# Kernel tuning notes

Measured on AMD Instinct MI355X. Metric: run time of the kernel, lower is better.

The kernel has to match this reference:

```python
import jax, jax.numpy as jnp
import numpy as np

WARMUP = 5

def _smooth_l1(x):
    a = jnp.abs(x)
    return jnp.where(a < 1.0, 0.5 * a * a, a - 0.5)


def setup_inputs() -> dict:
    key = jax.random.key(0)
    ks = jax.random.split(key, 6)
    B, S, N, M, C = 8, 4, 8192, 50, 10
    return dict(
        pred_boxes=jax.random.normal(ks[0], (B, S, N, 7), jnp.float32),
        pred_classes=jax.random.normal(ks[1], (B, S, N, C), jnp.float32),
        pred_scores=jax.random.normal(ks[2], (B, S, N), jnp.float32),
        gt_boxes=jax.random.normal(ks[3], (B, M, 7), jnp.float32) * 3.0,
        gt_classes=jax.random.randint(ks[4], (B, M), 0, C),
        n_gt=jax.random.randint(ks[5], (B,), 1, M + 1),
        w_center=jnp.float32(2.0),   # loss_weights['center']
        w_obj=jnp.float32(0.5),      # loss_weights['obj']
        w_unmatched=jnp.float32(5.0),# loss_weights['unmatched']
        epoch=0,
    )


def _forward(pred_boxes, pred_classes, pred_scores, gt_boxes, gt_classes, n_gt, w_center, w_obj, w_unmatched, epoch):
    # epoch < WARMUP path: k_factor=10, use_objectness=False, distance_threshold=5.0, cls_weight=0
    K_FACTOR = 10
    COST_THRESH = 5.0 * 10.0  # distance_threshold * 10
    B, S, N, _ = pred_boxes.shape
    M = gt_boxes.shape[1]
    gt_mask = jnp.arange(M)[None, :] < n_gt[:, None]            # [B,M] valid (non-padded) GTs

    pc = pred_boxes[..., :3]                                    # [B,S,N,3]
    gc = gt_boxes[..., :3]                                      # [B,M,3]
    diff = pc[:, :, :, None, :] - gc[:, None, None, :, :]       # [B,S,N,M,3]
    dist = jnp.sqrt(jnp.sum(diff * diff, axis=-1))              # [B,S,N,M] center L2 cost

    # ---- progressive matching (vectorized over B,S,GT) ----
    cost = jnp.where(gt_mask[:, None, None, :], dist, jnp.inf)
    masked = jnp.where(cost < COST_THRESH, cost, jnp.inf)
    neg = -jnp.swapaxes(masked, -1, -2)                         # [B,S,M,N]
    vals, idx = jax.lax.top_k(neg, K_FACTOR)                    # k smallest costs per gt
    pick_ok = vals > -jnp.inf                                   # [B,S,M,k] valid picks
    gt_ids = jnp.broadcast_to(jnp.arange(M, dtype=jnp.int32)[None, None, :, None], idx.shape)
    bidx = jnp.broadcast_to(jnp.arange(B)[:, None, None, None], idx.shape)
    sidx = jnp.broadcast_to(jnp.arange(S)[None, :, None, None], idx.shape)
    assign = jnp.full((B, S, N), -1, dtype=jnp.int32)
    assign = assign.at[bidx, sidx, idx].max(jnp.where(pick_ok, gt_ids, -1))
    matched_gt = pick_ok.any(-1)                                # [B,S,M]
    unmatched = gt_mask[:, None, :] & ~matched_gt               # [B,S,M]

    # ---- center loss (smooth-L1 over matched query/GT center pairs) ----
    pos = assign >= 0                                           # [B,S,N]
    a = jnp.maximum(assign, 0)
    gtc = gc[jnp.arange(B)[:, None, None], a]                   # [B,S,N,3]
    n_pos = pos.sum().astype(jnp.float32)
    loss_center = jnp.sum(_smooth_l1(pc - gtc) * pos[..., None]) / jnp.maximum(n_pos * 3.0, 1.0)

    # ---- progressive objectness loss (BCE-with-logits + dynamic pos_weight) ----
    t = pos.astype(pred_scores.dtype)
    n_neg = jnp.float32(t.size) - n_pos
    pw = jnp.minimum(10.0, n_neg / jnp.maximum(n_pos, 1.0))     # epoch < warmup branch
    x = pred_scores
    loss_obj = jnp.mean(pw * t * jax.nn.softplus(-x) + (1.0 - t) * jax.nn.softplus(x))

    # ---- unmatched-GT loss: pull 5 nearest predictions toward each unmatched GT ----
    dist_t = jnp.swapaxes(dist, -1, -2)                         # [B,S,M,N]
    nd, ni = jax.lax.top_k(-dist_t, 5)
    nd = -nd                                                    # 5 smallest distances [B,S,M,5]
    b5 = jnp.broadcast_to(jnp.arange(B)[:, None, None, None], ni.shape)
    s5 = jnp.broadcast_to(jnp.arange(S)[None, :, None, None], ni.shape)
    obj5 = pred_scores[b5, s5, ni]                              # [B,S,M,5]
    per_gt = jnp.mean(jnp.exp(-nd / 2.0) * (1.0 - obj5), axis=-1)
    per_gt = jnp.where(unmatched, per_gt, 0.0)
    n_entries = jnp.sum(unmatched.any(-1)).astype(jnp.float32)  # number of (b,s) pairs with unmatched gts
    loss_unm = per_gt.sum() / jnp.maximum(n_entries, 1.0)

    return loss_center * w_center + loss_obj * w_obj + loss_unm * w_unmatched


def reference(pred_boxes, pred_classes, pred_scores, gt_boxes, gt_classes, n_gt, w_center, w_obj, w_unmatched, epoch):
    return _forward(pred_boxes, pred_classes, pred_scores, gt_boxes, gt_classes, n_gt, w_center, w_obj, w_unmatched, epoch)
```

## Files before the change

kernel.cpp:

```cpp
#include <hip/hip_runtime.h>

#define NB 8
#define NS 4
#define NN 8192
#define NM 50
#define K10 10
#define THREADS 256
#define COST_THRESH 50.0f
#define LOSS_BLOCKS 256
#define NBUCK 1024
#define CAP 256
#define TOTAL (NB * NS * NN)

__device__ __forceinline__ bool lexless(float d1, int i1, float d2, int i2) {
  return (d1 < d2) || (d1 == d2 && i1 < i2);
}

__global__ void __launch_bounds__(256) prep_kernel(
    const float* __restrict__ pred_boxes, float* __restrict__ packed,
    int* __restrict__ assign, float* __restrict__ acc,
    int* __restrict__ bs_unm, int* __restrict__ done) {
  int i = blockIdx.x * blockDim.x + threadIdx.x;
  for (int j = i; j < TOTAL; j += gridDim.x * blockDim.x) {
    assign[j] = -1;
    packed[j] = pred_boxes[j * 7 + 0];
    packed[TOTAL + j] = pred_boxes[j * 7 + 1];
    packed[2 * TOTAL + j] = pred_boxes[j * 7 + 2];
  }
  if (i == 0) { acc[0] = 0.0f; *done = 0; }
  if (i >= 64 && i < 64 + NB * NS) bs_unm[i - 64] = 0;
}

__global__ void __launch_bounds__(256) topk_kernel(
    const float* __restrict__ packed, const float* __restrict__ pred_scores,
    const float* __restrict__ gt_boxes, const int* __restrict__ n_gt,
    int* __restrict__ assign, float* __restrict__ per_gt_sum,
    int* __restrict__ bs_unm) {
  const int blk = blockIdx.x;
  const int m = blk % NM;
  const int bs = blk / NM;
  const int b = bs / NS;
  const int t = threadIdx.x;

  __shared__ float sd2[NN];
  __shared__ int shist[NBUCK];
  __shared__ float scd[CAP];
  __shared__ int sci[CAP];
  __shared__ float sred[16];
  __shared__ float sbb[2];
  __shared__ int scnt;
  __shared__ int sbucket;
  __shared__ float soutd[K10];
  __shared__ int souti[K10];

  for (int i = t; i < NBUCK; i += THREADS) shist[i] = 0;
  if (t == 0) { scnt = 0; sbucket = NBUCK - 2; }

  const float gx = gt_boxes[(b * NM + m) * 7 + 0];
  const float gy = gt_boxes[(b * NM + m) * 7 + 1];
  const float gz = gt_boxes[(b * NM + m) * 7 + 2];
  const bool valid = (m < n_gt[b]);

  const float* px = packed + (size_t)bs * NN;
  const float* py = px + TOTAL;
  const float* pz = py + TOTAL;

  float lmin = INFINITY, lmax = 0.0f;
#pragma unroll
  for (int k = 0; k < NN / THREADS; k++) {
    int n = t + k * THREADS;
    float dx = px[n] - gx;
    float dy = py[n] - gy;
    float dz = pz[n] - gz;
    float d2 = dx * dx + dy * dy + dz * dz;
    sd2[n] = d2;
    lmin = fminf(lmin, d2);
    lmax = fmaxf(lmax, d2);
  }
#pragma unroll
  for (int off = 32; off >= 1; off >>= 1) {
    lmin = fminf(lmin, __shfl_down(lmin, off));
    lmax = fmaxf(lmax, __shfl_down(lmax, off));
  }
  int wave = t >> 6;
  if ((t & 63) == 0) { sred[wave] = lmin; sred[8 + wave] = lmax; }
  __syncthreads();
  if (t == 0) {
    float bmin = fminf(fminf(sred[0], sred[1]), fminf(sred[2], sred[3]));
    float bmax = fmaxf(fmaxf(sred[8], sred[9]), fmaxf(sred[10], sred[11]));
    sbb[0] = bmin;
    sbb[1] = (float)NBUCK / fmaxf(bmax - bmin, 1e-30f);
  }
  __syncthreads();
  const float bmin = sbb[0], scale = sbb[1];

#pragma unroll
  for (int k = 0; k < NN / THREADS; k++) {
    int n = t + k * THREADS;
    int bidx = (int)((sd2[n] - bmin) * scale);
    bidx = min(NBUCK - 1, max(0, bidx));
    atomicAdd(&shist[bidx], 1);
  }
  __syncthreads();

  if (t < 64) {
    int lsum = 0;
    for (int i = 0; i < NBUCK / 64; i++) lsum += shist[t * (NBUCK / 64) + i];
    int incl = lsum;
#pragma unroll
    for (int off = 1; off < 64; off <<= 1) {
      int v = __shfl_up(incl, off);
      if (t >= off) incl += v;
    }
    int excl = incl - lsum;
    if (excl < K10 && incl >= K10) {
      int c = excl;
      for (int i = 0; i < NBUCK / 64; i++) {
        c += shist[t * (NBUCK / 64) + i];
        if (c >= K10) { sbucket = t * (NBUCK / 64) + i; break; }
      }
    }
  }
  __syncthreads();
  const float bound = bmin + ((float)(sbucket + 2) + 0.5f) / scale;

#pragma unroll
  for (int k = 0; k < NN / THREADS; k++) {
    int n = t + k * THREADS;
    float d2 = sd2[n];
    if (d2 < bound) {
      int p = atomicAdd(&scnt, 1);
      if (p < CAP) { scd[p] = d2; sci[p] = n; }
    }
  }
  __syncthreads();
  const int K = min(scnt, CAP);

  for (int c = t; c < K; c += THREADS) scd[c] = sqrtf(scd[c]);
  __syncthreads();
  for (int c = t; c < K; c += THREADS) {
    float dc = scd[c];
    int ic = sci[c];
    int rank = 0;
    for (int o = 0; o < K; o++) rank += lexless(scd[o], sci[o], dc, ic) ? 1 : 0;
    if (rank < K10) { soutd[rank] = dc; souti[rank] = ic; }
  }
  __syncthreads();

  if (t < 64) {
    bool pick = (t < K10) && valid && (soutd[t] < COST_THRESH);
    if (pick) atomicMax(&assign[(size_t)bs * NN + souti[t]], m);
    bool matched = __any(pick);
    if (valid && !matched) {
      float a = 0.0f;
      if (t < 5) a = expf(-0.5f * soutd[t]) * (1.0f - pred_scores[(size_t)bs * NN + souti[t]]);
#pragma unroll
      for (int off = 8; off >= 1; off >>= 1) a += __shfl_down(a, off);
      if (t == 0) {
        atomicAdd(per_gt_sum, a * 0.2f);
        atomicOr(&bs_unm[bs], 1);
      }
    }
  }
}

__global__ void __launch_bounds__(256) loss_final_kernel(
    const float* __restrict__ packed, const float* __restrict__ pred_scores,
    const float* __restrict__ gt_boxes, const int* __restrict__ assign,
    float* __restrict__ partials, int* __restrict__ done,
    const float* __restrict__ acc, const int* __restrict__ bs_unm,
    const float* __restrict__ wc, const float* __restrict__ wo,
    const float* __restrict__ wu, float* __restrict__ out) {
  int tid = blockIdx.x * blockDim.x + threadIdx.x;
  float lc = 0.0f, spp = 0.0f, spn = 0.0f, np = 0.0f;
  for (int i = tid; i < TOTAL; i += gridDim.x * blockDim.x) {
    int a = assign[i];
    float x = pred_scores[i];
    if (a >= 0) {
      np += 1.0f;
      int b = i / (NS * NN);
      const float* gbp = &gt_boxes[(b * NM + a) * 7];
#pragma unroll
      for (int c = 0; c < 3; c++) {
        float diff = packed[c * TOTAL + i] - gbp[c];
        float ad = fabsf(diff);
        lc += (ad < 1.0f) ? 0.5f * ad * ad : (ad - 0.5f);
      }
      spp += log1pf(expf(-fabsf(x))) + fmaxf(-x, 0.0f);
    } else {
      spn += log1pf(expf(-fabsf(x))) + fmaxf(x, 0.0f);
    }
  }
#pragma unroll
  for (int off = 32; off >= 1; off >>= 1) {
    lc += __shfl_down(lc, off);
    spp += __shfl_down(spp, off);
    spn += __shfl_down(spn, off);
    np += __shfl_down(np, off);
  }
  __shared__ float red[4][4];
  __shared__ int s_last;
  int wave = threadIdx.x >> 6;
  if ((threadIdx.x & 63) == 0) {
    red[wave][0] = lc; red[wave][1] = spp; red[wave][2] = spn; red[wave][3] = np;
  }
  __syncthreads();
  if (threadIdx.x == 0) {
    float o0 = 0, o1 = 0, o2 = 0, o3 = 0;
#pragma unroll
    for (int w = 0; w < 4; w++) { o0 += red[w][0]; o1 += red[w][1]; o2 += red[w][2]; o3 += red[w][3]; }
    float* p = &partials[(size_t)blockIdx.x * 8];
    __hip_atomic_store(&p[0], o0, __ATOMIC_RELAXED, __HIP_MEMORY_SCOPE_AGENT);
    __hip_atomic_store(&p[1], o1, __ATOMIC_RELAXED, __HIP_MEMORY_SCOPE_AGENT);
    __hip_atomic_store(&p[2], o2, __ATOMIC_RELAXED, __HIP_MEMORY_SCOPE_AGENT);
    __hip_atomic_store(&p[3], o3, __ATOMIC_RELAXED, __HIP_MEMORY_SCOPE_AGENT);
    __threadfence();
    int ticket = __hip_atomic_fetch_add(done, 1, __ATOMIC_ACQ_REL, __HIP_MEMORY_SCOPE_AGENT);
    s_last = (ticket == gridDim.x - 1) ? 1 : 0;
  }
  __syncthreads();
  if (s_last) {
    __threadfence();
    const int t = threadIdx.x;
    float l0 = __hip_atomic_load(&partials[t * 8 + 0], __ATOMIC_RELAXED, __HIP_MEMORY_SCOPE_AGENT);
    float l1 = __hip_atomic_load(&partials[t * 8 + 1], __ATOMIC_RELAXED, __HIP_MEMORY_SCOPE_AGENT);
    float l2 = __hip_atomic_load(&partials[t * 8 + 2], __ATOMIC_RELAXED, __HIP_MEMORY_SCOPE_AGENT);
    float l3 = __hip_atomic_load(&partials[t * 8 + 3], __ATOMIC_RELAXED, __HIP_MEMORY_SCOPE_AGENT);
#pragma unroll
    for (int off = 32; off >= 1; off >>= 1) {
      l0 += __shfl_down(l0, off);
      l1 += __shfl_down(l1, off);
      l2 += __shfl_down(l2, off);
      l3 += __shfl_down(l3, off);
    }
    __shared__ float red2[4][4];
    if ((t & 63) == 0) {
      red2[t >> 6][0] = l0; red2[t >> 6][1] = l1; red2[t >> 6][2] = l2; red2[t >> 6][3] = l3;
    }
    __syncthreads();
    if (t == 0) {
      float o0 = 0, o1 = 0, o2 = 0, o3 = 0;
#pragma unroll
      for (int w = 0; w < 4; w++) { o0 += red2[w][0]; o1 += red2[w][1]; o2 += red2[w][2]; o3 += red2[w][3]; }
      int ne = 0;
      for (int i = 0; i < NB * NS; i++) ne += bs_unm[i];
      float n_pos = o3;
      float loss_center = o0 / fmaxf(n_pos * 3.0f, 1.0f);
      float n_neg = (float)TOTAL - n_pos;
      float pw = fminf(10.0f, n_neg / fmaxf(n_pos, 1.0f));
      float loss_obj = (pw * o1 + o2) / (float)TOTAL;
      float loss_unm = acc[0] / fmaxf((float)ne, 1.0f);
      out[0] = loss_center * wc[0] + loss_obj * wo[0] + loss_unm * wu[0];
    }
  }
}

extern "C" void kernel_launch(void* const* d_in, const int* in_sizes, int n_in,
                              void* d_out, int out_size, void* d_ws, size_t ws_size,
                              hipStream_t stream) {
  const float* pred_boxes = (const float*)d_in[0];
  const float* pred_scores = (const float*)d_in[2];
  const float* gt_boxes = (const float*)d_in[3];
  const int* n_gt = (const int*)d_in[5];
  const float* wc = (const float*)d_in[6];
  const float* wo = (const float*)d_in[7];
  const float* wu = (const float*)d_in[8];
  float* out = (float*)d_out;

  char* ws = (char*)d_ws;
  int* assign = (int*)ws;
  float* packed = (float*)(ws + (size_t)TOTAL * 4);
  float* acc = (float*)(ws + (size_t)TOTAL * 16);
  int* done = (int*)((char*)acc + 64);
  int* bs_unm = (int*)((char*)acc + 128);
  float* partials = (float*)((char*)acc + 512);

  prep_kernel<<<512, 256, 0, stream>>>(pred_boxes, packed, assign, acc, bs_unm, done);
  topk_kernel<<<NB * NS * NM, THREADS, 0, stream>>>(packed, pred_scores, gt_boxes,
                                                    n_gt, assign, &acc[0], bs_unm);
  loss_final_kernel<<<LOSS_BLOCKS, 256, 0, stream>>>(packed, pred_scores, gt_boxes, assign,
                                                     partials, done, acc, bs_unm, wc, wo, wu, out);
}
```

Baseline: 48.15 us.

## Keep distances in registers, vectorize loads, use 512 threads and sub-histograms

The top-k kernel now keeps per-thread squared distances in registers instead of a 32KB shared array, loads coordinates as float4, runs with 512 threads per block, and spreads histogram atomics over four per-wave sub-histograms that are merged before the prefix scan. This removes the large shared-memory footprint that limited occupancy and cuts atomic contention on the histogram. The cost is register pressure from 16 live distances per thread plus an extra merge pass and barrier. Candidate indices are recomputed from the float4 layout, and the final rank loop is unchanged.

```diff
diff --git a/kernel.cpp b/kernel.cpp
--- a/kernel.cpp
+++ b/kernel.cpp
@@ -5,12 +5,14 @@
 #define NN 8192
 #define NM 50
 #define K10 10
-#define THREADS 256
 #define COST_THRESH 50.0f
 #define LOSS_BLOCKS 256
 #define NBUCK 1024
+#define NSUB 4
 #define CAP 256
 #define TOTAL (NB * NS * NN)
+#define TT 512
+#define ELEMS (NN / TT)
 
 __device__ __forceinline__ bool lexless(float d1, int i1, float d2, int i2) {
   return (d1 < d2) || (d1 == d2 && i1 < i2);
@@ -31,7 +33,7 @@
   if (i >= 64 && i < 64 + NB * NS) bs_unm[i - 64] = 0;
 }
 
-__global__ void __launch_bounds__(256) topk_kernel(
+__global__ void __launch_bounds__(TT) topk_kernel(
     const float* __restrict__ packed, const float* __restrict__ pred_scores,
     const float* __restrict__ gt_boxes, const int* __restrict__ n_gt,
     int* __restrict__ assign, float* __restrict__ per_gt_sum,
@@ -42,8 +44,7 @@
   const int b = bs / NS;
   const int t = threadIdx.x;
 
-  __shared__ float sd2[NN];
-  __shared__ int shist[NBUCK];
+  __shared__ int shist[NSUB][NBUCK];
   __shared__ float scd[CAP];
   __shared__ int sci[CAP];
   __shared__ float sred[16];
@@ -53,7 +54,7 @@
   __shared__ float soutd[K10];
   __shared__ int souti[K10];
 
-  for (int i = t; i < NBUCK; i += THREADS) shist[i] = 0;
+  for (int i = t; i < NSUB * NBUCK; i += TT) ((int*)shist)[i] = 0;
   if (t == 0) { scnt = 0; sbucket = NBUCK - 2; }
 
   const float gx = gt_boxes[(b * NM + m) * 7 + 0];
@@ -61,51 +62,64 @@
   const float gz = gt_boxes[(b * NM + m) * 7 + 2];
   const bool valid = (m < n_gt[b]);
 
-  const float* px = packed + (size_t)bs * NN;
-  const float* py = px + TOTAL;
-  const float* pz = py + TOTAL;
-
+  const float4* px4 = (const float4*)(packed + (size_t)bs * NN);
+  const float4* py4 = (const float4*)(packed + TOTAL + (size_t)bs * NN);
+  const float4* pz4 = (const float4*)(packed + 2 * TOTAL + (size_t)bs * NN);
+
+  float d2r[ELEMS];
   float lmin = INFINITY, lmax = 0.0f;
 #pragma unroll
-  for (int k = 0; k < NN / THREADS; k++) {
-    int n = t + k * THREADS;
-    float dx = px[n] - gx;
-    float dy = py[n] - gy;
-    float dz = pz[n] - gz;
-    float d2 = dx * dx + dy * dy + dz * dz;
-    sd2[n] = d2;
-    lmin = fminf(lmin, d2);
-    lmax = fmaxf(lmax, d2);
+  for (int c = 0; c < ELEMS / 4; c++) {
+    float4 vx = px4[c * TT + t];
+    float4 vy = py4[c * TT + t];
+    float4 vz = pz4[c * TT + t];
+    float dx, dy, dz;
+    dx = vx.x - gx; dy = vy.x - gy; dz = vz.x - gz; d2r[c * 4 + 0] = dx * dx + dy * dy + dz * dz;
+    dx = vx.y - gx; dy = vy.y - gy; dz = vz.y - gz; d2r[c * 4 + 1] = dx * dx + dy * dy + dz * dz;
+    dx = vx.z - gx; dy = vy.z - gy; dz = vz.z - gz; d2r[c * 4 + 2] = dx * dx + dy * dy + dz * dz;
+    dx = vx.w - gx; dy = vy.w - gy; dz = vz.w - gz; d2r[c * 4 + 3] = dx * dx + dy * dy + dz * dz;
+#pragma unroll
+    for (int j = 0; j < 4; j++) {
+      lmin = fminf(lmin, d2r[c * 4 + j]);
+      lmax = fmaxf(lmax, d2r[c * 4 + j]);
+    }
   }
 #pragma unroll
   for (int off = 32; off >= 1; off >>= 1) {
     lmin = fminf(lmin, __shfl_down(lmin, off));
     lmax = fmaxf(lmax, __shfl_down(lmax, off));
   }
-  int wave = t >> 6;
+  const int wave = t >> 6;
   if ((t & 63) == 0) { sred[wave] = lmin; sred[8 + wave] = lmax; }
   __syncthreads();
   if (t == 0) {
-    float bmin = fminf(fminf(sred[0], sred[1]), fminf(sred[2], sred[3]));
-    float bmax = fmaxf(fmaxf(sred[8], sred[9]), fmaxf(sred[10], sred[11]));
+    float bmin = INFINITY, bmax = 0.0f;
+#pragma unroll
+    for (int w = 0; w < TT / 64; w++) {
+      bmin = fminf(bmin, sred[w]);
+      bmax = fmaxf(bmax, sred[8 + w]);
+    }
     sbb[0] = bmin;
     sbb[1] = (float)NBUCK / fmaxf(bmax - bmin, 1e-30f);
   }
   __syncthreads();
   const float bmin = sbb[0], scale = sbb[1];
 
-#pragma unroll
-  for (int k = 0; k < NN / THREADS; k++) {
-    int n = t + k * THREADS;
-    int bidx = (int)((sd2[n] - bmin) * scale);
+  int* hist = shist[wave & (NSUB - 1)];
+#pragma unroll
+  for (int e = 0; e < ELEMS; e++) {
+    int bidx = (int)((d2r[e] - bmin) * scale);
     bidx = min(NBUCK - 1, max(0, bidx));
-    atomicAdd(&shist[bidx], 1);
-  }
+    atomicAdd(&hist[bidx], 1);
+  }
+  __syncthreads();
+  for (int i = t; i < NBUCK; i += TT)
+    shist[0][i] += shist[1][i] + shist[2][i] + shist[3][i];
   __syncthreads();
 
   if (t < 64) {
     int lsum = 0;
-    for (int i = 0; i < NBUCK / 64; i++) lsum += shist[t * (NBUCK / 64) + i];
+    for (int i = 0; i < NBUCK / 64; i++) lsum += shist[0][t * (NBUCK / 64) + i];
     int incl = lsum;
 #pragma unroll
     for (int off = 1; off < 64; off <<= 1) {
@@ -116,7 +130,7 @@
     if (excl < K10 && incl >= K10) {
       int c = excl;
       for (int i = 0; i < NBUCK / 64; i++) {
-        c += shist[t * (NBUCK / 64) + i];
+        c += shist[0][t * (NBUCK / 64) + i];
         if (c >= K10) { sbucket = t * (NBUCK / 64) + i; break; }
       }
     }
@@ -125,20 +139,22 @@
   const float bound = bmin + ((float)(sbucket + 2) + 0.5f) / scale;
 
 #pragma unroll
-  for (int k = 0; k < NN / THREADS; k++) {
-    int n = t + k * THREADS;
-    float d2 = sd2[n];
-    if (d2 < bound) {
-      int p = atomicAdd(&scnt, 1);
-      if (p < CAP) { scd[p] = d2; sci[p] = n; }
+  for (int c = 0; c < ELEMS / 4; c++) {
+#pragma unroll
+    for (int j = 0; j < 4; j++) {
+      float d2 = d2r[c * 4 + j];
+      if (d2 < bound) {
+        int p = atomicAdd(&scnt, 1);
+        if (p < CAP) { scd[p] = d2; sci[p] = (c * TT + t) * 4 + j; }
+      }
     }
   }
   __syncthreads();
   const int K = min(scnt, CAP);
 
-  for (int c = t; c < K; c += THREADS) scd[c] = sqrtf(scd[c]);
-  __syncthreads();
-  for (int c = t; c < K; c += THREADS) {
+  for (int c = t; c < K; c += TT) scd[c] = sqrtf(scd[c]);
+  __syncthreads();
+  for (int c = t; c < K; c += TT) {
     float dc = scd[c];
     int ic = sci[c];
     int rank = 0;
@@ -276,8 +292,8 @@
   float* partials = (float*)((char*)acc + 512);
 
   prep_kernel<<<512, 256, 0, stream>>>(pred_boxes, packed, assign, acc, bs_unm, done);
-  topk_kernel<<<NB * NS * NM, THREADS, 0, stream>>>(packed, pred_scores, gt_boxes,
-                                                    n_gt, assign, &acc[0], bs_unm);
+  topk_kernel<<<NB * NS * NM, TT, 0, stream>>>(packed, pred_scores, gt_boxes,
+                                               n_gt, assign, &acc[0], bs_unm);
   loss_final_kernel<<<LOSS_BLOCKS, 256, 0, stream>>>(packed, pred_scores, gt_boxes, assign,
                                                      partials, done, acc, bs_unm, wc, wo, wu, out);
 }
```

After: 46.49 us. -3.4%, faster.
